# Performance work log

Measured on AMD Instinct MI355X. Metric: run time of the kernel, lower is better.

The kernel has to match this reference:

```python
import jax, jax.numpy as jnp
import numpy as np

N_LAYERS = 4
EPS = 1e-5  # eqx.nn.LayerNorm default


def _kernels(lam, P, B, C, step, L):
    # Annotated-S4 DPLR generating-function kernel (Q = P), vectorized over H channels.
    # lam, P, B, C: (H, N) complex64; step: (H, 1) real. Returns K: (H, L) real.
    omega = jnp.exp((-2j * jnp.pi) * (jnp.arange(L) / L))            # (L,) roots of unity
    g = (2.0 / step) * ((1.0 - omega) / (1.0 + omega))[None, :]      # (H, L) bilinear warp
    c = 2.0 / (1.0 + omega)                                          # (L,)

    def cauchy(v):  # v: (H, N) -> (H, L): sum_n v_n / (g - lambda_n)
        return jnp.sum(v[:, None, :] / (g[:, :, None] - lam[:, None, :]), axis=-1)

    k00 = cauchy(jnp.conj(C) * B)
    k01 = cauchy(jnp.conj(C) * P)
    k10 = cauchy(jnp.conj(P) * B)
    k11 = cauchy(jnp.conj(P) * P)
    at_roots = c[None, :] * (k00 - k01 * (1.0 / (1.0 + k11)) * k10)  # woodbury correction
    return jnp.fft.ifft(at_roots, n=L, axis=-1).real                 # (H, L)


def _causal_conv(u, K):
    # u: (B, L, H) real input, K: (H, L) real kernel -> causal conv along L via zero-padded FFT.
    L = u.shape[1]
    Ud = jnp.fft.rfft(u, n=2 * L, axis=1)                 # (B, F, H)
    Kd = jnp.fft.rfft(K, n=2 * L, axis=-1)                # (H, F)
    return jnp.fft.irfft(Ud * Kd.T[None], n=2 * L, axis=1)[:, :L]


def _forward(x, enc_w, enc_b, dec_w, dec_b, lam_re, lam_im, p_re, p_im, b_re, b_im,
             c_re, c_im, d, log_step, norm_w, norm_b, w1, b1, w2, b2):
    L = x.shape[1]
    h = x @ enc_w.T + enc_b                               # encoder: (B, L, H)
    for i in range(N_LAYERS):
        skip = h
        mu = h.mean(-1, keepdims=True)
        var = ((h - mu) ** 2).mean(-1, keepdims=True)
        hn = (h - mu) / jnp.sqrt(var + EPS) * norm_w[i] + norm_b[i]
        K = _kernels(lam_re[i] + 1j * lam_im[i], p_re[i] + 1j * p_im[i],
                     b_re[i] + 1j * b_im[i], c_re[i] + 1j * c_im[i],
                     jnp.exp(log_step[i])[:, None], L)
        y = _causal_conv(hn, K) + hn * d[i]               # SSM conv + skip-through D term
        y = jax.nn.gelu(y)
        y = (y @ w1[i].T + b1[i]) * jax.nn.sigmoid(y @ w2[i].T + b2[i])  # gated MLP
        h = skip + y
    return h @ dec_w.T + dec_b                            # decoder: (B, L, out)


def setup_inputs() -> dict:
    key = jax.random.key(0)
    B, L, IN, OUT, H, N, NL = 8, 2048, 64, 64, 128, 64, N_LAYERS
    ks = jax.random.split(key, 12)
    rn = lambda k, s, sc: (jax.random.normal(k, s) * sc).astype(jnp.float32)
    return dict(
        x=rn(ks[0], (B, L, IN), 1.0),
        convolve=1,
        enc_w=rn(ks[1], (H, IN), 1.0 / np.sqrt(IN)), enc_b=jnp.zeros((H,), jnp.float32),
        dec_w=rn(ks[2], (OUT, H), 1.0 / np.sqrt(H)), dec_b=jnp.zeros((OUT,), jnp.float32),
        lam_re=-0.5 * jnp.ones((NL, H, N), jnp.float32),  # HiPPO/S4D-style stable poles
        lam_im=jnp.tile(jnp.float32(np.pi) * jnp.arange(N, dtype=jnp.float32), (NL, H, 1)),
        p_re=rn(ks[3], (NL, H, N), 0.5 / np.sqrt(N)), p_im=rn(ks[4], (NL, H, N), 0.5 / np.sqrt(N)),
        b_re=rn(ks[5], (NL, H, N), 1.0), b_im=rn(ks[6], (NL, H, N), 1.0),
        c_re=rn(ks[7], (NL, H, N), 1.0 / np.sqrt(N)), c_im=rn(ks[8], (NL, H, N), 1.0 / np.sqrt(N)),
        d=jnp.ones((NL, H), jnp.float32),
        log_step=(jax.random.uniform(ks[9], (NL, H)) * (np.log(0.1) - np.log(0.001))
                  + np.log(0.001)).astype(jnp.float32),
        norm_w=jnp.ones((NL, H), jnp.float32), norm_b=jnp.zeros((NL, H), jnp.float32),
        w1=rn(ks[10], (NL, H, H), 1.0 / np.sqrt(H)), b1=jnp.zeros((NL, H), jnp.float32),
        w2=rn(ks[11], (NL, H, H), 1.0 / np.sqrt(H)), b2=jnp.zeros((NL, H), jnp.float32),
    )


def reference(x, convolve, enc_w, enc_b, dec_w, dec_b, lam_re, lam_im, p_re, p_im,
              b_re, b_im, c_re, c_im, d, log_step, norm_w, norm_b, w1, b1, w2, b2):
    # convolve is static 1 (True): the FFT-convolution path of the S4 Model.
    return _forward(x, enc_w, enc_b, dec_w, dec_b, lam_re, lam_im, p_re, p_im, b_re, b_im,
                    c_re, c_im, d, log_step, norm_w, norm_b, w1, b1, w2, b2)
```

## Files before the change

### kernel.cpp

```cpp
#include <hip/hip_runtime.h>
#include <hip/hip_bf16.h>


#define Bsz 8
#define Lseq 2048
#define Hdim 128
#define Npol 64
#define NLAYERS 4

typedef __bf16 bf16x8 __attribute__((ext_vector_type(8)));
typedef float f32x16 __attribute__((ext_vector_type(16)));

__device__ __forceinline__ float fast_rcp(float x) { return __builtin_amdgcn_rcpf(x); }
__device__ __forceinline__ float fast_rsq(float x) { return __builtin_amdgcn_rsqf(x); }

__device__ __forceinline__ float2 cmulf(float2 a, float2 b) {
    return make_float2(a.x * b.x - a.y * b.y, a.x * b.y + a.y * b.x);
}
__device__ __forceinline__ float2 cmulc(float2 a, float2 b) {
    return make_float2(a.x * b.x + a.y * b.y, a.y * b.x - a.x * b.y);
}

__device__ __forceinline__ float gelu_f(float v) {
    float z = 0.7978845608028654f * (v + 0.044715f * v * v * v);
    float e = __expf(2.0f * z);
    return v - v * fast_rcp(e + 1.0f);
}

__device__ __forceinline__ int sw(int i) { return (i & ~15) | ((i ^ (i >> 4)) & 15); }

static __device__ const float W16R[8] = {1.f, 0.9238795325f, 0.7071067812f, 0.3826834324f,
                                         0.f, -0.3826834324f, -0.7071067812f, -0.9238795325f};
static __device__ const float W16I[8] = {0.f, -0.3826834324f, -0.7071067812f, -0.9238795325f,
                                         -1.f, -0.9238795325f, -0.7071067812f, -0.3826834324f};
static __device__ const int BR4[16] = {0, 8, 4, 12, 2, 10, 6, 14, 1, 9, 5, 13, 3, 11, 7, 15};
static __device__ const int BR3[8] = {0, 4, 2, 6, 1, 5, 3, 7};

__device__ __forceinline__ float2 twget(const float2* __restrict__ tw, int e) {
    float2 w = tw[e & 2047];
    if (e & 2048) { w.x = -w.x; w.y = -w.y; }
    return w;
}

template <bool INV>
__device__ __forceinline__ void fft16_dif(float2 v[16]) {
#pragma unroll
    for (int mi = 0; mi < 4; mi++) {
        const int m = 8 >> mi;
#pragma unroll
        for (int g = 0; g < 16; g += 2 * m) {
#pragma unroll
            for (int j = 0; j < m; j++) {
                float wr = W16R[j << mi];
                float wi = INV ? -W16I[j << mi] : W16I[j << mi];
                float2 a = v[g + j], b = v[g + j + m];
                float dx = a.x - b.x, dy = a.y - b.y;
                v[g + j] = make_float2(a.x + b.x, a.y + b.y);
                v[g + j + m] = make_float2(dx * wr - dy * wi, dx * wi + dy * wr);
            }
        }
    }
}

template <bool INV>
__device__ __forceinline__ void fft16_dit(float2 v[16]) {
#pragma unroll
    for (int mi = 3; mi >= 0; mi--) {
        const int m = 8 >> mi;
#pragma unroll
        for (int g = 0; g < 16; g += 2 * m) {
#pragma unroll
            for (int j = 0; j < m; j++) {
                float wr = W16R[j << mi];
                float wi = INV ? -W16I[j << mi] : W16I[j << mi];
                float2 a = v[g + j], b = v[g + j + m];
                float bx = b.x * wr - b.y * wi, by = b.x * wi + b.y * wr;
                v[g + j] = make_float2(a.x + bx, a.y + by);
                v[g + j + m] = make_float2(a.x - bx, a.y - by);
            }
        }
    }
}

template <bool INV>
__device__ __forceinline__ void fft8_dif(float2 v[8]) {
#pragma unroll
    for (int mi = 0; mi < 3; mi++) {
        const int m = 4 >> mi;
#pragma unroll
        for (int g = 0; g < 8; g += 2 * m) {
#pragma unroll
            for (int j = 0; j < m; j++) {
                float wr = W16R[j << (mi + 1)];
                float wi = INV ? -W16I[j << (mi + 1)] : W16I[j << (mi + 1)];
                float2 a = v[g + j], b = v[g + j + m];
                float dx = a.x - b.x, dy = a.y - b.y;
                v[g + j] = make_float2(a.x + b.x, a.y + b.y);
                v[g + j + m] = make_float2(dx * wr - dy * wi, dx * wi + dy * wr);
            }
        }
    }
}

__device__ __forceinline__ void fft4096_fwd(float2* data, const float2* __restrict__ tw, int t) {
    {
        float2 v[16];
#pragma unroll
        for (int k = 0; k < 16; k++) v[k] = data[sw(t + 256 * k)];
        fft16_dif<false>(v);
#pragma unroll
        for (int i = 1; i < 16; i++) v[i] = cmulf(v[i], twget(tw, t * BR4[i]));
#pragma unroll
        for (int i = 0; i < 16; i++) data[sw(i * 256 + t)] = v[i];
    }
    __syncthreads();
    {
        int j0 = t & 15;
        int base = (t >> 4) * 256 + j0;
        float2 v[16];
#pragma unroll
        for (int k = 0; k < 16; k++) v[k] = data[sw(base + 16 * k)];
        fft16_dif<false>(v);
#pragma unroll
        for (int i = 1; i < 16; i++) v[i] = cmulf(v[i], twget(tw, 16 * j0 * BR4[i]));
#pragma unroll
        for (int i = 0; i < 16; i++) data[sw(base + 16 * i)] = v[i];
    }
    __syncthreads();
    {
        float2 v[16];
#pragma unroll
        for (int k = 0; k < 16; k++) v[k] = data[sw(t * 16 + k)];
        fft16_dif<false>(v);
#pragma unroll
        for (int i = 0; i < 16; i++) data[sw(t * 16 + i)] = v[i];
    }
    __syncthreads();
}

__global__ __launch_bounds__(256) void twiddle_init(float2* tw) {
    int k = blockIdx.x * blockDim.x + threadIdx.x;
    if (k < 2048) {
        double a = -6.283185307179586476925286766559 * (double)k / 4096.0;
        tw[k] = make_float2((float)cos(a), (float)sin(a));
    }
}

__global__ __launch_bounds__(256) void wtobf_kernel(const float* __restrict__ w1,
                                                    const float* __restrict__ w2,
                                                    __bf16* __restrict__ wbf) {
    int i = blockIdx.x * 256 + threadIdx.x;
    int layer = i >> 14, rem = i & 16383;
    wbf[((size_t)layer * 2) * 16384 + rem] = (__bf16)w1[i];
    wbf[((size_t)layer * 2 + 1) * 16384 + rem] = (__bf16)w2[i];
}

__global__ __launch_bounds__(256) void encoder_kernel(const float* __restrict__ x,
                                                      const float* __restrict__ w,
                                                      const float* __restrict__ b,
                                                      const float* __restrict__ nw,
                                                      const float* __restrict__ nb,
                                                      float* __restrict__ h,
                                                      float* __restrict__ hnT) {
    int r0 = blockIdx.x * 16;
    int t = threadIdx.x;
    __shared__ float ws[128 * 65];
    __shared__ __align__(16) float xst[64 * 20];
    __shared__ float dots[16 * 128];
    __shared__ float2 mv[16];
    for (int i = t; i < 128 * 64; i += 256) ws[(i >> 6) * 65 + (i & 63)] = w[i];
    for (int i = t; i < 16 * 64; i += 256) {
        int r = i >> 6, k = i & 63;
        xst[k * 20 + r] = x[(size_t)(r0 + r) * 64 + k];
    }
    __syncthreads();
    int o = t & 127, half = t >> 7;
    float acc[8];
    float bo = b[o];
#pragma unroll
    for (int j = 0; j < 8; j++) acc[j] = bo;
    for (int k = 0; k < 64; k++) {
        float wv = ws[o * 65 + k];
        float4 xa = *(const float4*)&xst[k * 20 + half * 8];
        float4 xb = *(const float4*)&xst[k * 20 + half * 8 + 4];
        acc[0] += wv * xa.x; acc[1] += wv * xa.y; acc[2] += wv * xa.z; acc[3] += wv * xa.w;
        acc[4] += wv * xb.x; acc[5] += wv * xb.y; acc[6] += wv * xb.z; acc[7] += wv * xb.w;
    }
#pragma unroll
    for (int j = 0; j < 8; j++) dots[(half * 8 + j) * 128 + o] = acc[j];
    __syncthreads();
    {
        int row = t >> 4, lane = t & 15;
        float s1 = 0.f, s2 = 0.f;
#pragma unroll
        for (int i = 0; i < 8; i++) {
            float v = dots[row * 128 + lane * 8 + i];
            s1 += v; s2 += v * v;
        }
#pragma unroll
        for (int m = 1; m < 16; m <<= 1) { s1 += __shfl_xor(s1, m); s2 += __shfl_xor(s2, m); }
        if (lane == 0) {
            float mu = s1 * (1.0f / 128.0f);
            float var = s2 * (1.0f / 128.0f) - mu * mu;
            mv[row] = make_float2(mu, fast_rsq(var + 1e-5f));
        }
    }
    __syncthreads();
    int c = t & 127;
    int bb = r0 >> 11, l0 = r0 & 2047;
    float nwc = nw[c], nbc = nb[c];
    float hnv[8];
#pragma unroll
    for (int j = 0; j < 8; j++) {
        int r = half * 8 + j;
        float v = dots[r * 128 + c];
        h[(size_t)(r0 + r) * Hdim + c] = v;
        float2 m = mv[r];
        hnv[j] = (v - m.x) * m.y * nwc + nbc;
    }
    float* dst = hnT + ((size_t)bb * Hdim + c) * Lseq + l0 + half * 8;
    *(float4*)dst = make_float4(hnv[0], hnv[1], hnv[2], hnv[3]);
    *(float4*)(dst + 4) = make_float4(hnv[4], hnv[5], hnv[6], hnv[7]);
}

__global__ __launch_bounds__(256, 4) void spectrum_kernel(const float* __restrict__ lam_re,
                                                          const float* __restrict__ lam_im,
                                                          const float* __restrict__ p_re,
                                                          const float* __restrict__ p_im,
                                                          const float* __restrict__ b_re,
                                                          const float* __restrict__ b_im,
                                                          const float* __restrict__ c_re,
                                                          const float* __restrict__ c_im,
                                                          const float* __restrict__ log_step,
                                                          float2* __restrict__ at_roots) {
    int h = blockIdx.x, layer = blockIdx.y, t = threadIdx.x;
    __shared__ __align__(16) float4 polA[Npol];
    __shared__ __align__(16) float4 polB[Npol];
    __shared__ float n11S[Npol];
    int baseP = (layer * Hdim + h) * Npol;
    if (t < Npol) {
        int n = t;
        float lr = lam_re[baseP + n], li = lam_im[baseP + n];
        float pr = p_re[baseP + n], pi = p_im[baseP + n];
        float br = b_re[baseP + n], bi = b_im[baseP + n];
        float cr = c_re[baseP + n], ci = c_im[baseP + n];
        polA[n] = make_float4(lr, li, cr * br + ci * bi, cr * bi - ci * br);
        polB[n] = make_float4(cr * pr + ci * pi, cr * pi - ci * pr,
                              pr * br + pi * bi, pr * bi - pi * br);
        n11S[n] = pr * pr + pi * pi;
    }
    __syncthreads();
    float step = expf(log_step[layer * Hdim + h]);
    float gs = 2.0f / step;
    int l0 = 512 * blockIdx.z;

    float gr[2], gi[2];
#pragma unroll
    for (int j = 0; j < 2; j++) {
        int l = l0 + t + 256 * j;
        float ang = -6.283185307179586f * (float)l / (float)Lseq;
        float wr = cosf(ang), wi = sinf(ang);
        float dr = 1.0f + wr, di = wi;
        float invd2 = fast_rcp(dr * dr + di * di);
        float nr = 1.0f - wr, ni = -wi;
        gr[j] = gs * (nr * dr + ni * di) * invd2;
        gi[j] = gs * (ni * dr - nr * di) * invd2;
    }
    float k00x[2] = {0, 0}, k00y[2] = {0, 0};
    float k01x[2] = {0, 0}, k01y[2] = {0, 0};
    float k10x[2] = {0, 0}, k10y[2] = {0, 0};
    float k11x[2] = {0, 0}, k11y[2] = {0, 0};
#pragma unroll 4
    for (int n = 0; n < Npol; n++) {
        float4 A = polA[n];
        float4 B = polB[n];
        float n11 = n11S[n];
#pragma unroll
        for (int j = 0; j < 2; j++) {
            float er = gr[j] - A.x, ei = gi[j] - A.y;
            float inv2 = fast_rcp(fmaf(er, er, ei * ei));
            float ir = er * inv2;
            float mi = ei * inv2;
            k00x[j] = fmaf(A.z, ir, fmaf(A.w, mi, k00x[j]));
            k00y[j] = fmaf(A.w, ir, fmaf(-A.z, mi, k00y[j]));
            k01x[j] = fmaf(B.x, ir, fmaf(B.y, mi, k01x[j]));
            k01y[j] = fmaf(B.y, ir, fmaf(-B.x, mi, k01y[j]));
            k10x[j] = fmaf(B.z, ir, fmaf(B.w, mi, k10x[j]));
            k10y[j] = fmaf(B.w, ir, fmaf(-B.z, mi, k10y[j]));
            k11x[j] = fmaf(n11, ir, k11x[j]);
            k11y[j] = fmaf(-n11, mi, k11y[j]);
        }
    }
#pragma unroll
    for (int j = 0; j < 2; j++) {
        int l = l0 + t + 256 * j;
        float ang = -6.283185307179586f * (float)l / (float)Lseq;
        float wr = cosf(ang), wi = sinf(ang);
        float dr = 1.0f + wr, di = wi;
        float invd2 = fast_rcp(dr * dr + di * di);
        float cr2 = 2.0f * dr * invd2, ci2 = -2.0f * di * invd2;
        float wr2 = 1.0f + k11x[j], wi2 = k11y[j];
        float w2inv = fast_rcp(fmaf(wr2, wr2, wi2 * wi2));
        float vr = wr2 * w2inv, vi = -wi2 * w2inv;
        float t1x = k01x[j] * k10x[j] - k01y[j] * k10y[j];
        float t1y = k01x[j] * k10y[j] + k01y[j] * k10x[j];
        float t2x = t1x * vr - t1y * vi, t2y = t1x * vi + t1y * vr;
        float ex = k00x[j] - t2x, ey = k00y[j] - t2y;
        at_roots[((size_t)layer * Hdim + h) * Lseq + l] =
            make_float2(cr2 * ex - ci2 * ey, cr2 * ey + ci2 * ex);
    }
}

__global__ __launch_bounds__(256) void kfft_kernel(const float2* __restrict__ at_roots,
                                                   float4* __restrict__ Kd2,
                                                   const float2* __restrict__ tw) {
    int h = blockIdx.x, layer = blockIdx.y, t = threadIdx.x;
    __shared__ float2 data[4096];
    __shared__ float ktmp[2048];
    const float2* src = at_roots + ((size_t)layer * Hdim + h) * Lseq;
#pragma unroll
    for (int k = 0; k < 8; k++) {
        int l = t + 256 * k;
        data[sw(l)] = src[l];
    }
    __syncthreads();
    if (t < 128) {
        float2 v[16];
#pragma unroll
        for (int k = 0; k < 16; k++) v[k] = data[sw(t + 128 * k)];
        fft16_dif<true>(v);
#pragma unroll
        for (int i = 1; i < 16; i++) v[i] = cmulc(v[i], twget(tw, 2 * t * BR4[i]));
#pragma unroll
        for (int i = 0; i < 16; i++) data[sw(i * 128 + t)] = v[i];
    }
    __syncthreads();
    if (t < 128) {
        int i2 = t >> 3, j0 = t & 7;
        int base2 = i2 * 128 + j0;
        float2 v[16];
#pragma unroll
        for (int k = 0; k < 16; k++) v[k] = data[sw(base2 + 8 * k)];
        fft16_dif<true>(v);
#pragma unroll
        for (int i = 1; i < 16; i++) v[i] = cmulc(v[i], twget(tw, 32 * j0 * BR4[i]));
#pragma unroll
        for (int i = 0; i < 16; i++) data[sw(base2 + 8 * i)] = v[i];
    }
    __syncthreads();
    {
        float2 v8[8];
#pragma unroll
        for (int k = 0; k < 8; k++) v8[k] = data[sw(t * 8 + k)];
        fft8_dif<true>(v8);
        int r = BR4[t >> 4], s = BR4[t & 15];
#pragma unroll
        for (int i = 0; i < 8; i++) {
            int l = r + 16 * s + 256 * BR3[i];
            ktmp[l] = v8[i].x * (1.0f / 2048.0f);
        }
    }
    __syncthreads();
#pragma unroll
    for (int k = 0; k < 8; k++) {
        int l = t + 256 * k;
        data[sw(l)] = make_float2(ktmp[l], 0.f);
        data[sw(l + 2048)] = make_float2(0.f, 0.f);
    }
    fft4096_fwd(data, tw, t);
    float2* dst = (float2*)(Kd2 + ((size_t)layer * 64 + (h >> 1)) * 4096);
    int half = h & 1;
#pragma unroll
    for (int k = 0; k < 16; k++) {
        int p = t + 256 * k;
        dst[2 * p + half] = data[sw(p)];
    }
}

__global__ __launch_bounds__(256) void conv_kernel(float* __restrict__ hnT,
                                                   const float4* __restrict__ Kd2,
                                                   const float* __restrict__ dvec,
                                                   const float2* __restrict__ tw) {
    int hp = blockIdx.x, b = blockIdx.y, h0 = hp * 2, t = threadIdx.x;
    __shared__ float2 data[4096];
    float* u0 = hnT + ((size_t)b * Hdim + h0) * Lseq;
    float* u1 = u0 + Lseq;
    float2 ureg[8];
#pragma unroll
    for (int k = 0; k < 8; k++) {
        int l = t + 256 * k;
        float2 u2 = make_float2(u0[l], u1[l]);
        ureg[k] = u2;
        data[sw(l)] = u2;
        data[sw(l + 2048)] = make_float2(0.f, 0.f);
    }
    fft4096_fwd(data, tw, t);
    const float4* Kp = Kd2 + (size_t)hp * 4096;
    const float scale = 1.0f / 4096.0f;
#pragma unroll
    for (int k = 0; k < 8; k++) {
        int p = 2 * (t + 256 * k);
        int f = __brev((unsigned)p) >> 20;
        int fm = (4096 - f) & 4095;
        int pm = __brev((unsigned)fm) >> 20;
        float2 Zf = data[sw(p)], Zm = data[sw(pm)];
        float2 U0 = make_float2(0.5f * (Zf.x + Zm.x), 0.5f * (Zf.y - Zm.y));
        float2 Dm = make_float2(Zf.x - Zm.x, Zf.y + Zm.y);
        float2 U1 = make_float2(0.5f * Dm.y, -0.5f * Dm.x);
        float4 Ka = Kp[p];
        float2 S0 = cmulf(U0, make_float2(Ka.x, Ka.y));
        float2 S1 = cmulf(U1, make_float2(Ka.z, Ka.w));
        float2 Wf = make_float2((S0.x - S1.y) * scale, (S0.y + S1.x) * scale);
        float4 Kb = Kp[pm];
        float2 U0m = make_float2(U0.x, -U0.y);
        float2 U1m = make_float2(U1.x, -U1.y);
        float2 S0m = cmulf(U0m, make_float2(Kb.x, Kb.y));
        float2 S1m = cmulf(U1m, make_float2(Kb.z, Kb.w));
        float2 Wm = make_float2((S0m.x - S1m.y) * scale, (S0m.y + S1m.x) * scale);
        data[sw(p)] = Wf;
        if (pm != p) data[sw(pm)] = Wm;
    }
    if (t == 0) {
        float2 Zf = data[sw(1)];
        float2 U0 = make_float2(Zf.x, 0.f);
        float2 U1 = make_float2(Zf.y, 0.f);
        float4 Ka = Kp[1];
        float2 S0 = cmulf(U0, make_float2(Ka.x, Ka.y));
        float2 S1 = cmulf(U1, make_float2(Ka.z, Ka.w));
        data[sw(1)] = make_float2((S0.x - S1.y) * scale, (S0.y + S1.x) * scale);
    }
    __syncthreads();
    {
        float2 v[16];
#pragma unroll
        for (int i = 0; i < 16; i++) v[i] = data[sw(t * 16 + i)];
        fft16_dit<true>(v);
#pragma unroll
        for (int i = 0; i < 16; i++) data[sw(t * 16 + i)] = v[i];
    }
    __syncthreads();
    {
        int j0 = t & 15;
        int base2 = (t >> 4) * 256 + j0;
        float2 v[16];
        v[0] = data[sw(base2)];
#pragma unroll
        for (int i = 1; i < 16; i++)
            v[i] = cmulc(data[sw(base2 + 16 * i)], twget(tw, 16 * j0 * BR4[i]));
        fft16_dit<true>(v);
#pragma unroll
        for (int i = 0; i < 16; i++) data[sw(base2 + 16 * i)] = v[i];
    }
    __syncthreads();
    {
        float2 v[16];
        v[0] = data[sw(t)];
#pragma unroll
        for (int i = 1; i < 16; i++)
            v[i] = cmulc(data[sw(i * 256 + t)], twget(tw, t * BR4[i]));
        fft16_dit<true>(v);
        float d0 = dvec[h0], d1 = dvec[h0 + 1];
#pragma unroll
        for (int k = 0; k < 8; k++) {
            int l = t + 256 * k;
            u0[l] = gelu_f(v[k].x + ureg[k].x * d0);
            u1[l] = gelu_f(v[k].y + ureg[k].y * d1);
        }
    }
}

__global__ __launch_bounds__(256) void mlp_kernel(const float* __restrict__ yT,
                                                  float* __restrict__ h,
                                                  float* __restrict__ hnT,
                                                  const __bf16* __restrict__ w1b,
                                                  const __bf16* __restrict__ w2b,
                                                  const float* __restrict__ b1,
                                                  const float* __restrict__ b2,
                                                  const float* __restrict__ nw,
                                                  const float* __restrict__ nb,
                                                  int do_ln) {
    int r0 = blockIdx.x * 32;
    int t = threadIdx.x;
    int wave = t >> 6, lane = t & 63;
    __shared__ __align__(16) __bf16 ybf[32 * 136];
    __shared__ float dots[32 * 132];
    __shared__ float2 mv[32];
    int bb = r0 >> 11, l0 = r0 & 2047;
    for (int i = t; i < 32 * 128; i += 256) {
        int r = i & 31, k = i >> 5;
        ybf[r * 136 + k] = (__bf16)yT[((size_t)bb * Hdim + k) * Lseq + l0 + r];
    }
    __syncthreads();
    int m = lane & 31, half = lane >> 5;
    bf16x8 a[8];
#pragma unroll
    for (int kk = 0; kk < 8; kk++)
        a[kk] = *(const bf16x8*)&ybf[m * 136 + kk * 16 + half * 8];
    int out = 32 * wave + m;
    const __bf16* w1r = w1b + (size_t)out * 128 + half * 8;
    const __bf16* w2r = w2b + (size_t)out * 128 + half * 8;
    f32x16 acc1, acc2;
#pragma unroll
    for (int i = 0; i < 16; i++) { acc1[i] = 0.f; acc2[i] = 0.f; }
#pragma unroll
    for (int kk = 0; kk < 8; kk++) {
        bf16x8 bw1 = *(const bf16x8*)(w1r + kk * 16);
        bf16x8 bw2 = *(const bf16x8*)(w2r + kk * 16);
        acc1 = __builtin_amdgcn_mfma_f32_32x32x16_bf16(a[kk], bw1, acc1, 0, 0, 0);
        acc2 = __builtin_amdgcn_mfma_f32_32x32x16_bf16(a[kk], bw2, acc2, 0, 0, 0);
    }
    float bias1 = b1[out], bias2 = b2[out];
#pragma unroll
    for (int reg = 0; reg < 16; reg++) {
        int row = (reg & 3) + 8 * (reg >> 2) + 4 * half;
        float v1 = acc1[reg] + bias1;
        float v2 = acc2[reg] + bias2;
        float g = fast_rcp(1.0f + __expf(-v2));
        float hv = h[(size_t)(r0 + row) * Hdim + out] + v1 * g;
        dots[row * 132 + out] = hv;
    }
    __syncthreads();
    if (do_ln) {
        int row = t >> 3, lane8 = t & 7;
        float s1 = 0.f, s2 = 0.f;
        int base = row * 132 + lane8 * 16;
#pragma unroll
        for (int q = 0; q < 4; q++) {
            float4 v4 = *(const float4*)&dots[base + 4 * q];
            s1 += v4.x + v4.y + v4.z + v4.w;
            s2 += v4.x * v4.x + v4.y * v4.y + v4.z * v4.z + v4.w * v4.w;
        }
#pragma unroll
        for (int mm = 1; mm < 8; mm <<= 1) { s1 += __shfl_xor(s1, mm); s2 += __shfl_xor(s2, mm); }
        if (lane8 == 0) {
            float mu = s1 * (1.0f / 128.0f);
            float var = s2 * (1.0f / 128.0f) - mu * mu;
            mv[row] = make_float2(mu, fast_rsq(var + 1e-5f));
        }
        __syncthreads();
        int o = t & 127, rh = t >> 7;
        float nwc = nw[o], nbc = nb[o];
        float hnv[16];
#pragma unroll
        for (int j = 0; j < 16; j++) {
            int r = rh * 16 + j;
            float hvv = dots[r * 132 + o];
            h[(size_t)(r0 + r) * Hdim + o] = hvv;
            float2 mvv = mv[r];
            hnv[j] = (hvv - mvv.x) * mvv.y * nwc + nbc;
        }
        float* dst = hnT + ((size_t)bb * Hdim + o) * Lseq + l0 + rh * 16;
        *(float4*)(dst)      = make_float4(hnv[0],  hnv[1],  hnv[2],  hnv[3]);
        *(float4*)(dst + 4)  = make_float4(hnv[4],  hnv[5],  hnv[6],  hnv[7]);
        *(float4*)(dst + 8)  = make_float4(hnv[8],  hnv[9],  hnv[10], hnv[11]);
        *(float4*)(dst + 12) = make_float4(hnv[12], hnv[13], hnv[14], hnv[15]);
    } else {
        int o = t & 127, rh = t >> 7;
#pragma unroll
        for (int j = 0; j < 16; j++) {
            int r = rh * 16 + j;
            h[(size_t)(r0 + r) * Hdim + o] = dots[r * 132 + o];
        }
    }
}

__global__ __launch_bounds__(256) void decoder_kernel(const float* __restrict__ h,
                                                      const float* __restrict__ w,
                                                      const float* __restrict__ b,
                                                      float* __restrict__ out) {
    int r0 = blockIdx.x * 32;
    int t = threadIdx.x;
    __shared__ float ws[64 * 129];
    __shared__ __align__(16) float hst[128 * 36];
    for (int i = t; i < 64 * 128; i += 256) ws[(i >> 7) * 129 + (i & 127)] = w[i];
    for (int i = t; i < 32 * 128; i += 256) {
        int r = i >> 7, k = i & 127;
        hst[k * 36 + r] = h[(size_t)(r0 + r) * Hdim + k];
    }
    __syncthreads();
    int o = t & 63, q = t >> 6;
    float acc[8];
    float bo = b[o];
#pragma unroll
    for (int j = 0; j < 8; j++) acc[j] = bo;
    for (int k = 0; k < 128; k++) {
        float wv = ws[o * 129 + k];
        float4 ha = *(const float4*)&hst[k * 36 + q * 8];
        float4 hb = *(const float4*)&hst[k * 36 + q * 8 + 4];
        acc[0] += wv * ha.x; acc[1] += wv * ha.y; acc[2] += wv * ha.z; acc[3] += wv * ha.w;
        acc[4] += wv * hb.x; acc[5] += wv * hb.y; acc[6] += wv * hb.z; acc[7] += wv * hb.w;
    }
#pragma unroll
    for (int j = 0; j < 8; j++) out[(size_t)(r0 + q * 8 + j) * 64 + o] = acc[j];
}

extern "C" void kernel_launch(void* const* d_in, const int* in_sizes, int n_in,
                              void* d_out, int out_size, void* d_ws, size_t ws_size,
                              hipStream_t stream) {
    const float* x      = (const float*)d_in[0];
    const float* enc_w  = (const float*)d_in[2];
    const float* enc_b  = (const float*)d_in[3];
    const float* dec_w  = (const float*)d_in[4];
    const float* dec_b  = (const float*)d_in[5];
    const float* lam_re = (const float*)d_in[6];
    const float* lam_im = (const float*)d_in[7];
    const float* p_re   = (const float*)d_in[8];
    const float* p_im   = (const float*)d_in[9];
    const float* b_re   = (const float*)d_in[10];
    const float* b_im   = (const float*)d_in[11];
    const float* c_re   = (const float*)d_in[12];
    const float* c_im   = (const float*)d_in[13];
    const float* dvec   = (const float*)d_in[14];
    const float* lstep  = (const float*)d_in[15];
    const float* norm_w = (const float*)d_in[16];
    const float* norm_b = (const float*)d_in[17];
    const float* w1     = (const float*)d_in[18];
    const float* b1     = (const float*)d_in[19];
    const float* w2     = (const float*)d_in[20];
    const float* b2     = (const float*)d_in[21];
    float* out = (float*)d_out;

    char* ws = (char*)d_ws;
    float2* tw  = (float2*)ws;  ws += 2048 * sizeof(float2);
    float*  h   = (float*)ws;   ws += (size_t)Bsz * Lseq * Hdim * sizeof(float);
    float*  hnT = (float*)ws;   ws += (size_t)Bsz * Lseq * Hdim * sizeof(float);
    float2* atr = (float2*)ws;  ws += (size_t)NLAYERS * Hdim * Lseq * sizeof(float2);
    float4* Kd2 = (float4*)ws;  ws += (size_t)NLAYERS * (Hdim / 2) * 4096 * sizeof(float4);
    __bf16* wbf = (__bf16*)ws;  ws += (size_t)NLAYERS * 2 * Hdim * Hdim * sizeof(__bf16);

    const int nrows = Bsz * Lseq;

    twiddle_init<<<8, 256, 0, stream>>>(tw);
    spectrum_kernel<<<dim3(Hdim, NLAYERS, 4), 256, 0, stream>>>(
        lam_re, lam_im, p_re, p_im, b_re, b_im, c_re, c_im, lstep, atr);
    kfft_kernel<<<dim3(Hdim, NLAYERS), 256, 0, stream>>>(atr, Kd2, tw);
    wtobf_kernel<<<256, 256, 0, stream>>>(w1, w2, wbf);
    encoder_kernel<<<nrows / 16, 256, 0, stream>>>(x, enc_w, enc_b, norm_w, norm_b, h, hnT);
    for (int L = 0; L < NLAYERS; L++) {
        conv_kernel<<<dim3(Hdim / 2, Bsz), 256, 0, stream>>>(
            hnT, Kd2 + (size_t)L * (Hdim / 2) * 4096, dvec + L * Hdim, tw);
        int do_ln = (L < NLAYERS - 1) ? 1 : 0;
        const float* nwn = norm_w + ((L + 1) % NLAYERS) * Hdim;
        const float* nbn = norm_b + ((L + 1) % NLAYERS) * Hdim;
        const __bf16* w1bL = wbf + (size_t)L * 2 * Hdim * Hdim;
        const __bf16* w2bL = w1bL + Hdim * Hdim;
        mlp_kernel<<<nrows / 32, 256, 0, stream>>>(hnT, h, hnT, w1bL, w2bL,
                                                   b1 + L * Hdim, b2 + L * Hdim,
                                                   nwn, nbn, do_ln);
    }
    decoder_kernel<<<nrows / 32, 256, 0, stream>>>(h, dec_w, dec_b, out);
}
```

Before: 325.5 us.

## Rewrite conv FFT as radix-8 four-pass with 512 threads and padded LDS

The 4096-point FFTs in the convolution kernel move from three radix-16 passes on 256 threads to four radix-8 passes on 512 threads. The XOR swizzle is replaced by a pad-one-every-16 shared-memory index to avoid bank conflicts. The aim is more threads per block and fewer registers per thread, which should help latency hiding on a grid of only 512 blocks. In exchange it adds an extra shared-memory pass and barrier per transform, plus slightly more LDS.

```diff
diff --git a/kernel.cpp b/kernel.cpp
--- a/kernel.cpp
+++ b/kernel.cpp
@@ -28,6 +28,7 @@
 }
 
 __device__ __forceinline__ int sw(int i) { return (i & ~15) | ((i ^ (i >> 4)) & 15); }
+__device__ __forceinline__ int ph(int i) { return i + (i >> 4); }
 
 static __device__ const float W16R[8] = {1.f, 0.9238795325f, 0.7071067812f, 0.3826834324f,
                                          0.f, -0.3826834324f, -0.7071067812f, -0.9238795325f};
@@ -63,26 +64,6 @@
 }
 
 template <bool INV>
-__device__ __forceinline__ void fft16_dit(float2 v[16]) {
-#pragma unroll
-    for (int mi = 3; mi >= 0; mi--) {
-        const int m = 8 >> mi;
-#pragma unroll
-        for (int g = 0; g < 16; g += 2 * m) {
-#pragma unroll
-            for (int j = 0; j < m; j++) {
-                float wr = W16R[j << mi];
-                float wi = INV ? -W16I[j << mi] : W16I[j << mi];
-                float2 a = v[g + j], b = v[g + j + m];
-                float bx = b.x * wr - b.y * wi, by = b.x * wi + b.y * wr;
-                v[g + j] = make_float2(a.x + bx, a.y + by);
-                v[g + j + m] = make_float2(a.x - bx, a.y - by);
-            }
-        }
-    }
-}
-
-template <bool INV>
 __device__ __forceinline__ void fft8_dif(float2 v[8]) {
 #pragma unroll
     for (int mi = 0; mi < 3; mi++) {
@@ -97,6 +78,26 @@
                 float dx = a.x - b.x, dy = a.y - b.y;
                 v[g + j] = make_float2(a.x + b.x, a.y + b.y);
                 v[g + j + m] = make_float2(dx * wr - dy * wi, dx * wi + dy * wr);
+            }
+        }
+    }
+}
+
+template <bool INV>
+__device__ __forceinline__ void fft8_dit(float2 v[8]) {
+#pragma unroll
+    for (int mi = 2; mi >= 0; mi--) {
+        const int m = 4 >> mi;
+#pragma unroll
+        for (int g = 0; g < 8; g += 2 * m) {
+#pragma unroll
+            for (int j = 0; j < m; j++) {
+                float wr = W16R[j << (mi + 1)];
+                float wi = INV ? -W16I[j << (mi + 1)] : W16I[j << (mi + 1)];
+                float2 a = v[g + j], b = v[g + j + m];
+                float bx = b.x * wr - b.y * wi, by = b.x * wi + b.y * wr;
+                v[g + j] = make_float2(a.x + bx, a.y + by);
+                v[g + j + m] = make_float2(a.x - bx, a.y - by);
             }
         }
     }
@@ -377,33 +378,77 @@
     }
 }
 
-__global__ __launch_bounds__(256) void conv_kernel(float* __restrict__ hnT,
+__global__ __launch_bounds__(512) void conv_kernel(float* __restrict__ hnT,
                                                    const float4* __restrict__ Kd2,
                                                    const float* __restrict__ dvec,
                                                    const float2* __restrict__ tw) {
     int hp = blockIdx.x, b = blockIdx.y, h0 = hp * 2, t = threadIdx.x;
-    __shared__ float2 data[4096];
+    __shared__ float2 data[4352];
     float* u0 = hnT + ((size_t)b * Hdim + h0) * Lseq;
     float* u1 = u0 + Lseq;
-    float2 ureg[8];
+    float2 ureg[4];
 #pragma unroll
     for (int k = 0; k < 8; k++) {
-        int l = t + 256 * k;
-        float2 u2 = make_float2(u0[l], u1[l]);
-        ureg[k] = u2;
-        data[sw(l)] = u2;
-        data[sw(l + 2048)] = make_float2(0.f, 0.f);
-    }
-    fft4096_fwd(data, tw, t);
+        int l = t + 512 * k;
+        float2 u2 = make_float2(0.f, 0.f);
+        if (k < 4) { u2 = make_float2(u0[l], u1[l]); ureg[k] = u2; }
+        data[ph(l)] = u2;
+    }
+    {
+        float2 v[8];
+#pragma unroll
+        for (int i = 0; i < 8; i++) v[i] = data[ph(t + 512 * i)];
+        fft8_dif<false>(v);
+#pragma unroll
+        for (int i = 1; i < 8; i++) v[i] = cmulf(v[i], twget(tw, t * BR3[i]));
+#pragma unroll
+        for (int i = 0; i < 8; i++) data[ph(t + 512 * i)] = v[i];
+    }
+    __syncthreads();
+    {
+        int blk = t >> 6, j = t & 63;
+        int base = 512 * blk + j;
+        float2 v[8];
+#pragma unroll
+        for (int i = 0; i < 8; i++) v[i] = data[ph(base + 64 * i)];
+        fft8_dif<false>(v);
+#pragma unroll
+        for (int i = 1; i < 8; i++) v[i] = cmulf(v[i], twget(tw, 8 * j * BR3[i]));
+#pragma unroll
+        for (int i = 0; i < 8; i++) data[ph(base + 64 * i)] = v[i];
+    }
+    __syncthreads();
+    {
+        int blk = t >> 3, j = t & 7;
+        int base = 64 * blk + j;
+        float2 v[8];
+#pragma unroll
+        for (int i = 0; i < 8; i++) v[i] = data[ph(base + 8 * i)];
+        fft8_dif<false>(v);
+#pragma unroll
+        for (int i = 1; i < 8; i++) v[i] = cmulf(v[i], twget(tw, 64 * j * BR3[i]));
+#pragma unroll
+        for (int i = 0; i < 8; i++) data[ph(base + 8 * i)] = v[i];
+    }
+    __syncthreads();
+    {
+        float2 v[8];
+#pragma unroll
+        for (int i = 0; i < 8; i++) v[i] = data[ph(8 * t + i)];
+        fft8_dif<false>(v);
+#pragma unroll
+        for (int i = 0; i < 8; i++) data[ph(8 * t + i)] = v[i];
+    }
+    __syncthreads();
     const float4* Kp = Kd2 + (size_t)hp * 4096;
     const float scale = 1.0f / 4096.0f;
 #pragma unroll
-    for (int k = 0; k < 8; k++) {
-        int p = 2 * (t + 256 * k);
+    for (int k = 0; k < 4; k++) {
+        int p = 2 * (t + 512 * k);
         int f = __brev((unsigned)p) >> 20;
         int fm = (4096 - f) & 4095;
         int pm = __brev((unsigned)fm) >> 20;
-        float2 Zf = data[sw(p)], Zm = data[sw(pm)];
+        float2 Zf = data[ph(p)], Zm = data[ph(pm)];
         float2 U0 = make_float2(0.5f * (Zf.x + Zm.x), 0.5f * (Zf.y - Zm.y));
         float2 Dm = make_float2(Zf.x - Zm.x, Zf.y + Zm.y);
         float2 U1 = make_float2(0.5f * Dm.y, -0.5f * Dm.x);
@@ -417,52 +462,65 @@
         float2 S0m = cmulf(U0m, make_float2(Kb.x, Kb.y));
         float2 S1m = cmulf(U1m, make_float2(Kb.z, Kb.w));
         float2 Wm = make_float2((S0m.x - S1m.y) * scale, (S0m.y + S1m.x) * scale);
-        data[sw(p)] = Wf;
-        if (pm != p) data[sw(pm)] = Wm;
+        data[ph(p)] = Wf;
+        if (pm != p) data[ph(pm)] = Wm;
     }
     if (t == 0) {
-        float2 Zf = data[sw(1)];
+        float2 Zf = data[ph(1)];
         float2 U0 = make_float2(Zf.x, 0.f);
         float2 U1 = make_float2(Zf.y, 0.f);
         float4 Ka = Kp[1];
         float2 S0 = cmulf(U0, make_float2(Ka.x, Ka.y));
         float2 S1 = cmulf(U1, make_float2(Ka.z, Ka.w));
-        data[sw(1)] = make_float2((S0.x - S1.y) * scale, (S0.y + S1.x) * scale);
-    }
-    __syncthreads();
-    {
-        float2 v[16];
-#pragma unroll
-        for (int i = 0; i < 16; i++) v[i] = data[sw(t * 16 + i)];
-        fft16_dit<true>(v);
-#pragma unroll
-        for (int i = 0; i < 16; i++) data[sw(t * 16 + i)] = v[i];
-    }
-    __syncthreads();
-    {
-        int j0 = t & 15;
-        int base2 = (t >> 4) * 256 + j0;
-        float2 v[16];
-        v[0] = data[sw(base2)];
-#pragma unroll
-        for (int i = 1; i < 16; i++)
-            v[i] = cmulc(data[sw(base2 + 16 * i)], twget(tw, 16 * j0 * BR4[i]));
-        fft16_dit<true>(v);
-#pragma unroll
-        for (int i = 0; i < 16; i++) data[sw(base2 + 16 * i)] = v[i];
-    }
-    __syncthreads();
-    {
-        float2 v[16];
-        v[0] = data[sw(t)];
-#pragma unroll
-        for (int i = 1; i < 16; i++)
-            v[i] = cmulc(data[sw(i * 256 + t)], twget(tw, t * BR4[i]));
-        fft16_dit<true>(v);
+        data[ph(1)] = make_float2((S0.x - S1.y) * scale, (S0.y + S1.x) * scale);
+    }
+    __syncthreads();
+    {
+        float2 v[8];
+#pragma unroll
+        for (int i = 0; i < 8; i++) v[i] = data[ph(8 * t + i)];
+        fft8_dit<true>(v);
+#pragma unroll
+        for (int i = 0; i < 8; i++) data[ph(8 * t + i)] = v[i];
+    }
+    __syncthreads();
+    {
+        int blk = t >> 3, j = t & 7;
+        int base = 64 * blk + j;
+        float2 v[8];
+        v[0] = data[ph(base)];
+#pragma unroll
+        for (int i = 1; i < 8; i++)
+            v[i] = cmulc(data[ph(base + 8 * i)], twget(tw, 64 * j * BR3[i]));
+        fft8_dit<true>(v);
+#pragma unroll
+        for (int i = 0; i < 8; i++) data[ph(base + 8 * i)] = v[i];
+    }
+    __syncthreads();
+    {
+        int blk = t >> 6, j = t & 63;
+        int base = 512 * blk + j;
+        float2 v[8];
+        v[0] = data[ph(base)];
+#pragma unroll
+        for (int i = 1; i < 8; i++)
+            v[i] = cmulc(data[ph(base + 64 * i)], twget(tw, 8 * j * BR3[i]));
+        fft8_dit<true>(v);
+#pragma unroll
+        for (int i = 0; i < 8; i++) data[ph(base + 64 * i)] = v[i];
+    }
+    __syncthreads();
+    {
+        float2 v[8];
+        v[0] = data[ph(t)];
+#pragma unroll
+        for (int i = 1; i < 8; i++)
+            v[i] = cmulc(data[ph(t + 512 * i)], twget(tw, t * BR3[i]));
+        fft8_dit<true>(v);
         float d0 = dvec[h0], d1 = dvec[h0 + 1];
 #pragma unroll
-        for (int k = 0; k < 8; k++) {
-            int l = t + 256 * k;
+        for (int k = 0; k < 4; k++) {
+            int l = t + 512 * k;
             u0[l] = gelu_f(v[k].x + ureg[k].x * d0);
             u1[l] = gelu_f(v[k].y + ureg[k].y * d1);
         }
@@ -637,7 +695,7 @@
     wtobf_kernel<<<256, 256, 0, stream>>>(w1, w2, wbf);
     encoder_kernel<<<nrows / 16, 256, 0, stream>>>(x, enc_w, enc_b, norm_w, norm_b, h, hnT);
     for (int L = 0; L < NLAYERS; L++) {
-        conv_kernel<<<dim3(Hdim / 2, Bsz), 256, 0, stream>>>(
+        conv_kernel<<<dim3(Hdim / 2, Bsz), 512, 0, stream>>>(
             hnT, Kd2 + (size_t)L * (Hdim / 2) * 4096, dvec + L * Hdim, tw);
         int do_ln = (L < NLAYERS - 1) ? 1 : 0;
         const float* nwn = norm_w + ((L + 1) % NLAYERS) * Hdim;
```

Result: no change. 328.3 us (+0.9%).

## Merge prep kernels, exploit zero-padding in FFT first pass, prune inverse last stage

Applied to the files above, without the earlier changes.

Merges twiddle init, weight bf16 conversion and spectrum computation into one launch, and folds the kernel FFT and the encoder into a second launch, so five launches become two and independent work can overlap. The first radix-16 pass of the 4096-point forward FFT now uses the fact that the upper half of the input is zero: it computes the first butterfly stage directly from eight register inputs and skips the shared-memory zero fill. The inverse FFT's final stage only computes the first eight outputs, since only the first half is kept. The merged kernels carry a larger shared-memory footprint and divergent block roles, which may lower occupancy for the smaller sub-tasks.

```diff
diff --git a/kernel.cpp b/kernel.cpp
--- a/kernel.cpp
+++ b/kernel.cpp
@@ -102,17 +102,36 @@
     }
 }
 
-__device__ __forceinline__ void fft4096_fwd(float2* data, const float2* __restrict__ tw, int t) {
-    {
-        float2 v[16];
-#pragma unroll
-        for (int k = 0; k < 16; k++) v[k] = data[sw(t + 256 * k)];
-        fft16_dif<false>(v);
-#pragma unroll
-        for (int i = 1; i < 16; i++) v[i] = cmulf(v[i], twget(tw, t * BR4[i]));
-#pragma unroll
-        for (int i = 0; i < 16; i++) data[sw(i * 256 + t)] = v[i];
-    }
+__device__ __forceinline__ void fft4096_passA_hz(float2* data, const float2* __restrict__ tw,
+                                                 int t, const float2 vin[8]) {
+    float2 v[16];
+#pragma unroll
+    for (int j = 0; j < 8; j++) v[j] = vin[j];
+#pragma unroll
+    for (int j = 0; j < 8; j++)
+        v[j + 8] = cmulf(v[j], make_float2(W16R[j], W16I[j]));
+#pragma unroll
+    for (int mi = 1; mi < 4; mi++) {
+        const int m = 8 >> mi;
+#pragma unroll
+        for (int g = 0; g < 16; g += 2 * m) {
+#pragma unroll
+            for (int j = 0; j < m; j++) {
+                float wr = W16R[j << mi], wi = W16I[j << mi];
+                float2 a = v[g + j], b = v[g + j + m];
+                float dx = a.x - b.x, dy = a.y - b.y;
+                v[g + j] = make_float2(a.x + b.x, a.y + b.y);
+                v[g + j + m] = make_float2(dx * wr - dy * wi, dx * wi + dy * wr);
+            }
+        }
+    }
+#pragma unroll
+    for (int i = 1; i < 16; i++) v[i] = cmulf(v[i], twget(tw, t * BR4[i]));
+#pragma unroll
+    for (int i = 0; i < 16; i++) data[sw(i * 256 + t)] = v[i];
+}
+
+__device__ __forceinline__ void fft4096_fwd_BC(float2* data, const float2* __restrict__ tw, int t) {
     __syncthreads();
     {
         int j0 = t & 15;
@@ -138,102 +157,39 @@
     __syncthreads();
 }
 
-__global__ __launch_bounds__(256) void twiddle_init(float2* tw) {
-    int k = blockIdx.x * blockDim.x + threadIdx.x;
-    if (k < 2048) {
-        double a = -6.283185307179586476925286766559 * (double)k / 4096.0;
-        tw[k] = make_float2((float)cos(a), (float)sin(a));
-    }
-}
-
-__global__ __launch_bounds__(256) void wtobf_kernel(const float* __restrict__ w1,
-                                                    const float* __restrict__ w2,
-                                                    __bf16* __restrict__ wbf) {
-    int i = blockIdx.x * 256 + threadIdx.x;
-    int layer = i >> 14, rem = i & 16383;
-    wbf[((size_t)layer * 2) * 16384 + rem] = (__bf16)w1[i];
-    wbf[((size_t)layer * 2 + 1) * 16384 + rem] = (__bf16)w2[i];
-}
-
-__global__ __launch_bounds__(256) void encoder_kernel(const float* __restrict__ x,
-                                                      const float* __restrict__ w,
-                                                      const float* __restrict__ b,
-                                                      const float* __restrict__ nw,
-                                                      const float* __restrict__ nb,
-                                                      float* __restrict__ h,
-                                                      float* __restrict__ hnT) {
-    int r0 = blockIdx.x * 16;
-    int t = threadIdx.x;
-    __shared__ float ws[128 * 65];
-    __shared__ __align__(16) float xst[64 * 20];
-    __shared__ float dots[16 * 128];
-    __shared__ float2 mv[16];
-    for (int i = t; i < 128 * 64; i += 256) ws[(i >> 6) * 65 + (i & 63)] = w[i];
-    for (int i = t; i < 16 * 64; i += 256) {
-        int r = i >> 6, k = i & 63;
-        xst[k * 20 + r] = x[(size_t)(r0 + r) * 64 + k];
-    }
-    __syncthreads();
-    int o = t & 127, half = t >> 7;
-    float acc[8];
-    float bo = b[o];
-#pragma unroll
-    for (int j = 0; j < 8; j++) acc[j] = bo;
-    for (int k = 0; k < 64; k++) {
-        float wv = ws[o * 65 + k];
-        float4 xa = *(const float4*)&xst[k * 20 + half * 8];
-        float4 xb = *(const float4*)&xst[k * 20 + half * 8 + 4];
-        acc[0] += wv * xa.x; acc[1] += wv * xa.y; acc[2] += wv * xa.z; acc[3] += wv * xa.w;
-        acc[4] += wv * xb.x; acc[5] += wv * xb.y; acc[6] += wv * xb.z; acc[7] += wv * xb.w;
-    }
-#pragma unroll
-    for (int j = 0; j < 8; j++) dots[(half * 8 + j) * 128 + o] = acc[j];
-    __syncthreads();
-    {
-        int row = t >> 4, lane = t & 15;
-        float s1 = 0.f, s2 = 0.f;
-#pragma unroll
-        for (int i = 0; i < 8; i++) {
-            float v = dots[row * 128 + lane * 8 + i];
-            s1 += v; s2 += v * v;
-        }
-#pragma unroll
-        for (int m = 1; m < 16; m <<= 1) { s1 += __shfl_xor(s1, m); s2 += __shfl_xor(s2, m); }
-        if (lane == 0) {
-            float mu = s1 * (1.0f / 128.0f);
-            float var = s2 * (1.0f / 128.0f) - mu * mu;
-            mv[row] = make_float2(mu, fast_rsq(var + 1e-5f));
-        }
-    }
-    __syncthreads();
-    int c = t & 127;
-    int bb = r0 >> 11, l0 = r0 & 2047;
-    float nwc = nw[c], nbc = nb[c];
-    float hnv[8];
-#pragma unroll
-    for (int j = 0; j < 8; j++) {
-        int r = half * 8 + j;
-        float v = dots[r * 128 + c];
-        h[(size_t)(r0 + r) * Hdim + c] = v;
-        float2 m = mv[r];
-        hnv[j] = (v - m.x) * m.y * nwc + nbc;
-    }
-    float* dst = hnT + ((size_t)bb * Hdim + c) * Lseq + l0 + half * 8;
-    *(float4*)dst = make_float4(hnv[0], hnv[1], hnv[2], hnv[3]);
-    *(float4*)(dst + 4) = make_float4(hnv[4], hnv[5], hnv[6], hnv[7]);
-}
-
-__global__ __launch_bounds__(256, 4) void spectrum_kernel(const float* __restrict__ lam_re,
-                                                          const float* __restrict__ lam_im,
-                                                          const float* __restrict__ p_re,
-                                                          const float* __restrict__ p_im,
-                                                          const float* __restrict__ b_re,
-                                                          const float* __restrict__ b_im,
-                                                          const float* __restrict__ c_re,
-                                                          const float* __restrict__ c_im,
-                                                          const float* __restrict__ log_step,
-                                                          float2* __restrict__ at_roots) {
-    int h = blockIdx.x, layer = blockIdx.y, t = threadIdx.x;
+__global__ __launch_bounds__(256, 4) void prep_kernel(const float* __restrict__ lam_re,
+                                                      const float* __restrict__ lam_im,
+                                                      const float* __restrict__ p_re,
+                                                      const float* __restrict__ p_im,
+                                                      const float* __restrict__ b_re,
+                                                      const float* __restrict__ b_im,
+                                                      const float* __restrict__ c_re,
+                                                      const float* __restrict__ c_im,
+                                                      const float* __restrict__ log_step,
+                                                      const float* __restrict__ w1,
+                                                      const float* __restrict__ w2,
+                                                      float2* __restrict__ tw,
+                                                      __bf16* __restrict__ wbf,
+                                                      float2* __restrict__ at_roots) {
+    int bid = blockIdx.x, t = threadIdx.x;
+    if (bid < 8) {
+        int k = bid * 256 + t;
+        if (k < 2048) {
+            double a = -6.283185307179586476925286766559 * (double)k / 4096.0;
+            tw[k] = make_float2((float)cos(a), (float)sin(a));
+        }
+        return;
+    }
+    if (bid < 264) {
+        int i = (bid - 8) * 256 + t;
+        int layer = i >> 14, rem = i & 16383;
+        wbf[((size_t)layer * 2) * 16384 + rem] = (__bf16)w1[i];
+        wbf[((size_t)layer * 2 + 1) * 16384 + rem] = (__bf16)w2[i];
+        return;
+    }
+    int s = bid - 264;
+    int h = s & 127, layer = (s >> 7) & 3;
+    int l0 = 512 * (s >> 9);
     __shared__ __align__(16) float4 polA[Npol];
     __shared__ __align__(16) float4 polB[Npol];
     __shared__ float n11S[Npol];
@@ -252,7 +208,6 @@
     __syncthreads();
     float step = expf(log_step[layer * Hdim + h]);
     float gs = 2.0f / step;
-    int l0 = 512 * blockIdx.z;
 
     float gr[2], gi[2];
 #pragma unroll
@@ -311,69 +266,139 @@
     }
 }
 
-__global__ __launch_bounds__(256) void kfft_kernel(const float2* __restrict__ at_roots,
-                                                   float4* __restrict__ Kd2,
-                                                   const float2* __restrict__ tw) {
-    int h = blockIdx.x, layer = blockIdx.y, t = threadIdx.x;
-    __shared__ float2 data[4096];
-    __shared__ float ktmp[2048];
-    const float2* src = at_roots + ((size_t)layer * Hdim + h) * Lseq;
-#pragma unroll
-    for (int k = 0; k < 8; k++) {
-        int l = t + 256 * k;
-        data[sw(l)] = src[l];
-    }
-    __syncthreads();
-    if (t < 128) {
-        float2 v[16];
-#pragma unroll
-        for (int k = 0; k < 16; k++) v[k] = data[sw(t + 128 * k)];
-        fft16_dif<true>(v);
-#pragma unroll
-        for (int i = 1; i < 16; i++) v[i] = cmulc(v[i], twget(tw, 2 * t * BR4[i]));
-#pragma unroll
-        for (int i = 0; i < 16; i++) data[sw(i * 128 + t)] = v[i];
-    }
-    __syncthreads();
-    if (t < 128) {
-        int i2 = t >> 3, j0 = t & 7;
-        int base2 = i2 * 128 + j0;
-        float2 v[16];
-#pragma unroll
-        for (int k = 0; k < 16; k++) v[k] = data[sw(base2 + 8 * k)];
-        fft16_dif<true>(v);
-#pragma unroll
-        for (int i = 1; i < 16; i++) v[i] = cmulc(v[i], twget(tw, 32 * j0 * BR4[i]));
-#pragma unroll
-        for (int i = 0; i < 16; i++) data[sw(base2 + 8 * i)] = v[i];
-    }
-    __syncthreads();
-    {
-        float2 v8[8];
-#pragma unroll
-        for (int k = 0; k < 8; k++) v8[k] = data[sw(t * 8 + k)];
-        fft8_dif<true>(v8);
-        int r = BR4[t >> 4], s = BR4[t & 15];
-#pragma unroll
-        for (int i = 0; i < 8; i++) {
-            int l = r + 16 * s + 256 * BR3[i];
-            ktmp[l] = v8[i].x * (1.0f / 2048.0f);
-        }
-    }
-    __syncthreads();
-#pragma unroll
-    for (int k = 0; k < 8; k++) {
-        int l = t + 256 * k;
-        data[sw(l)] = make_float2(ktmp[l], 0.f);
-        data[sw(l + 2048)] = make_float2(0.f, 0.f);
-    }
-    fft4096_fwd(data, tw, t);
-    float2* dst = (float2*)(Kd2 + ((size_t)layer * 64 + (h >> 1)) * 4096);
-    int half = h & 1;
-#pragma unroll
-    for (int k = 0; k < 16; k++) {
-        int p = t + 256 * k;
-        dst[2 * p + half] = data[sw(p)];
+__global__ __launch_bounds__(256) void kfft_enc_kernel(const float2* __restrict__ at_roots,
+                                                       float4* __restrict__ Kd2,
+                                                       const float2* __restrict__ tw,
+                                                       const float* __restrict__ x,
+                                                       const float* __restrict__ enc_w,
+                                                       const float* __restrict__ enc_b,
+                                                       const float* __restrict__ nw,
+                                                       const float* __restrict__ nb,
+                                                       float* __restrict__ h,
+                                                       float* __restrict__ hnT) {
+    __shared__ __align__(16) float smem[11712];
+    int bid = blockIdx.x, t = threadIdx.x;
+    if (bid < 512) {
+        int hh = bid & 127, layer = bid >> 7;
+        float2* data = (float2*)smem;
+        float* ktmp = smem + 8192;
+        const float2* src = at_roots + ((size_t)layer * Hdim + hh) * Lseq;
+#pragma unroll
+        for (int k = 0; k < 8; k++) {
+            int l = t + 256 * k;
+            data[sw(l)] = src[l];
+        }
+        __syncthreads();
+        if (t < 128) {
+            float2 v[16];
+#pragma unroll
+            for (int k = 0; k < 16; k++) v[k] = data[sw(t + 128 * k)];
+            fft16_dif<true>(v);
+#pragma unroll
+            for (int i = 1; i < 16; i++) v[i] = cmulc(v[i], twget(tw, 2 * t * BR4[i]));
+#pragma unroll
+            for (int i = 0; i < 16; i++) data[sw(i * 128 + t)] = v[i];
+        }
+        __syncthreads();
+        if (t < 128) {
+            int i2 = t >> 3, j0 = t & 7;
+            int base2 = i2 * 128 + j0;
+            float2 v[16];
+#pragma unroll
+            for (int k = 0; k < 16; k++) v[k] = data[sw(base2 + 8 * k)];
+            fft16_dif<true>(v);
+#pragma unroll
+            for (int i = 1; i < 16; i++) v[i] = cmulc(v[i], twget(tw, 32 * j0 * BR4[i]));
+#pragma unroll
+            for (int i = 0; i < 16; i++) data[sw(base2 + 8 * i)] = v[i];
+        }
+        __syncthreads();
+        {
+            float2 v8[8];
+#pragma unroll
+            for (int k = 0; k < 8; k++) v8[k] = data[sw(t * 8 + k)];
+            fft8_dif<true>(v8);
+            int r = BR4[t >> 4], s = BR4[t & 15];
+#pragma unroll
+            for (int i = 0; i < 8; i++) {
+                int l = r + 16 * s + 256 * BR3[i];
+                ktmp[l] = v8[i].x * (1.0f / 2048.0f);
+            }
+        }
+        __syncthreads();
+        {
+            float2 vin[8];
+#pragma unroll
+            for (int k = 0; k < 8; k++) vin[k] = make_float2(ktmp[t + 256 * k], 0.f);
+            fft4096_passA_hz(data, tw, t, vin);
+        }
+        fft4096_fwd_BC(data, tw, t);
+        float2* dst = (float2*)(Kd2 + ((size_t)layer * 64 + (hh >> 1)) * 4096);
+        int half = hh & 1;
+#pragma unroll
+        for (int k = 0; k < 16; k++) {
+            int p = t + 256 * k;
+            dst[2 * p + half] = data[sw(p)];
+        }
+    } else {
+        int r0 = (bid - 512) * 16;
+        float* ws = smem;
+        float* xst = smem + 8320;
+        float* dots = smem + 9600;
+        float2* mv = (float2*)(smem + 11648);
+        for (int i = t; i < 128 * 64; i += 256) ws[(i >> 6) * 65 + (i & 63)] = enc_w[i];
+        for (int i = t; i < 16 * 64; i += 256) {
+            int r = i >> 6, k = i & 63;
+            xst[k * 20 + r] = x[(size_t)(r0 + r) * 64 + k];
+        }
+        __syncthreads();
+        int o = t & 127, half = t >> 7;
+        float acc[8];
+        float bo = enc_b[o];
+#pragma unroll
+        for (int j = 0; j < 8; j++) acc[j] = bo;
+        for (int k = 0; k < 64; k++) {
+            float wv = ws[o * 65 + k];
+            float4 xa = *(const float4*)&xst[k * 20 + half * 8];
+            float4 xb = *(const float4*)&xst[k * 20 + half * 8 + 4];
+            acc[0] += wv * xa.x; acc[1] += wv * xa.y; acc[2] += wv * xa.z; acc[3] += wv * xa.w;
+            acc[4] += wv * xb.x; acc[5] += wv * xb.y; acc[6] += wv * xb.z; acc[7] += wv * xb.w;
+        }
+#pragma unroll
+        for (int j = 0; j < 8; j++) dots[(half * 8 + j) * 128 + o] = acc[j];
+        __syncthreads();
+        {
+            int row = t >> 4, lane = t & 15;
+            float s1 = 0.f, s2 = 0.f;
+#pragma unroll
+            for (int i = 0; i < 8; i++) {
+                float v = dots[row * 128 + lane * 8 + i];
+                s1 += v; s2 += v * v;
+            }
+#pragma unroll
+            for (int m = 1; m < 16; m <<= 1) { s1 += __shfl_xor(s1, m); s2 += __shfl_xor(s2, m); }
+            if (lane == 0) {
+                float mu = s1 * (1.0f / 128.0f);
+                float var = s2 * (1.0f / 128.0f) - mu * mu;
+                mv[row] = make_float2(mu, fast_rsq(var + 1e-5f));
+            }
+        }
+        __syncthreads();
+        int c = t & 127;
+        int bb = r0 >> 11, l0 = r0 & 2047;
+        float nwc = nw[c], nbc = nb[c];
+        float hnv[8];
+#pragma unroll
+        for (int j = 0; j < 8; j++) {
+            int r = half * 8 + j;
+            float v = dots[r * 128 + c];
+            h[(size_t)(r0 + r) * Hdim + c] = v;
+            float2 m = mv[r];
+            hnv[j] = (v - m.x) * m.y * nwc + nbc;
+        }
+        float* dst = hnT + ((size_t)bb * Hdim + c) * Lseq + l0 + half * 8;
+        *(float4*)dst = make_float4(hnv[0], hnv[1], hnv[2], hnv[3]);
+        *(float4*)(dst + 4) = make_float4(hnv[4], hnv[5], hnv[6], hnv[7]);
     }
 }
 
@@ -386,15 +411,18 @@
     float* u0 = hnT + ((size_t)b * Hdim + h0) * Lseq;
     float* u1 = u0 + Lseq;
     float2 ureg[8];
-#pragma unroll
-    for (int k = 0; k < 8; k++) {
-        int l = t + 256 * k;
-        float2 u2 = make_float2(u0[l], u1[l]);
-        ureg[k] = u2;
-        data[sw(l)] = u2;
-        data[sw(l + 2048)] = make_float2(0.f, 0.f);
-    }
-    fft4096_fwd(data, tw, t);
+    {
+        float2 vin[8];
+#pragma unroll
+        for (int k = 0; k < 8; k++) {
+            int l = t + 256 * k;
+            float2 u2 = make_float2(u0[l], u1[l]);
+            ureg[k] = u2;
+            vin[k] = u2;
+        }
+        fft4096_passA_hz(data, tw, t, vin);
+    }
+    fft4096_fwd_BC(data, tw, t);
     const float4* Kp = Kd2 + (size_t)hp * 4096;
     const float scale = 1.0f / 4096.0f;
 #pragma unroll
@@ -458,7 +486,28 @@
 #pragma unroll
         for (int i = 1; i < 16; i++)
             v[i] = cmulc(data[sw(i * 256 + t)], twget(tw, t * BR4[i]));
-        fft16_dit<true>(v);
+#pragma unroll
+        for (int mi = 3; mi >= 1; mi--) {
+            const int m = 8 >> mi;
+#pragma unroll
+            for (int g = 0; g < 16; g += 2 * m) {
+#pragma unroll
+                for (int j = 0; j < m; j++) {
+                    float wr = W16R[j << mi], wi = -W16I[j << mi];
+                    float2 a = v[g + j], bb2 = v[g + j + m];
+                    float bx = bb2.x * wr - bb2.y * wi, by = bb2.x * wi + bb2.y * wr;
+                    v[g + j] = make_float2(a.x + bx, a.y + by);
+                    v[g + j + m] = make_float2(a.x - bx, a.y - by);
+                }
+            }
+        }
+#pragma unroll
+        for (int j = 0; j < 8; j++) {
+            float wr = W16R[j], wi = -W16I[j];
+            float2 bb2 = v[j + 8];
+            float bx = bb2.x * wr - bb2.y * wi, by = bb2.x * wi + bb2.y * wr;
+            v[j] = make_float2(v[j].x + bx, v[j].y + by);
+        }
         float d0 = dvec[h0], d1 = dvec[h0 + 1];
 #pragma unroll
         for (int k = 0; k < 8; k++) {
@@ -630,12 +679,10 @@
 
     const int nrows = Bsz * Lseq;
 
-    twiddle_init<<<8, 256, 0, stream>>>(tw);
-    spectrum_kernel<<<dim3(Hdim, NLAYERS, 4), 256, 0, stream>>>(
-        lam_re, lam_im, p_re, p_im, b_re, b_im, c_re, c_im, lstep, atr);
-    kfft_kernel<<<dim3(Hdim, NLAYERS), 256, 0, stream>>>(atr, Kd2, tw);
-    wtobf_kernel<<<256, 256, 0, stream>>>(w1, w2, wbf);
-    encoder_kernel<<<nrows / 16, 256, 0, stream>>>(x, enc_w, enc_b, norm_w, norm_b, h, hnT);
+    prep_kernel<<<8 + 256 + 2048, 256, 0, stream>>>(
+        lam_re, lam_im, p_re, p_im, b_re, b_im, c_re, c_im, lstep, w1, w2, tw, wbf, atr);
+    kfft_enc_kernel<<<512 + nrows / 16, 256, 0, stream>>>(
+        atr, Kd2, tw, x, enc_w, enc_b, norm_w, norm_b, h, hnT);
     for (int L = 0; L < NLAYERS; L++) {
         conv_kernel<<<dim3(Hdim / 2, Bsz), 256, 0, stream>>>(
             hnT, Kd2 + (size_t)L * (Hdim / 2) * 4096, dvec + L * Hdim, tw);
```

Result: faster. 311.7 us (-4.2%).
